# Kernel tuning notes

Measured on AMD Instinct MI355X. Metric: run time of the kernel, lower is better.

Reference implementation:

```python
import jax, jax.numpy as jnp
import numpy as np

N = 80000        # nodes
E = 1280000      # edges (avg degree 16)
D_IN, H1, H2, D_OUT = 64, 64, 64, 64


def _glorot(key, fan_in, fan_out):
    s = np.sqrt(6.0 / (fan_in + fan_out)).astype(np.float32)
    return jax.random.uniform(key, (fan_in, fan_out), jnp.float32, -s, s)


def setup_inputs() -> dict:
    key = jax.random.key(0)
    ks = jax.random.split(key, 5)
    X = jax.random.normal(ks[0], (N, D_IN), jnp.float32)
    edge_index = jax.random.randint(ks[1], (2, E), 0, N, dtype=jnp.int32).astype(jnp.int64)
    W1 = _glorot(ks[2], D_IN, H1)
    W2 = _glorot(ks[3], H1, H2)
    W3 = _glorot(ks[4], H2, D_OUT)
    b1 = jnp.zeros((H1,), jnp.float32)
    b2 = jnp.zeros((H2,), jnp.float32)
    b3 = jnp.zeros((D_OUT,), jnp.float32)
    return {"X": X, "edge_index": edge_index,
            "W1": W1, "b1": b1, "W2": W2, "b2": b2, "W3": W3, "b3": b3}


def _gcn_conv(x, W, b, src, dst, n):
    """PyG GCNConv: symmetric-normalized mean over A + I, then linear + bias.
    x' = D^{-1/2} (A + I) D^{-1/2} (x W) + b, deg counts self-loops."""
    x = x @ W                                   # [N, F_out]
    # in-degree including self loop (edge weights are 1)
    deg = jnp.ones((n,), x.dtype).at[dst].add(1.0)
    dinv = jax.lax.rsqrt(deg)                   # deg >= 1 always
    coef = dinv[src] * dinv[dst]                # [E]
    msg = x[src] * coef[:, None]                # [E, F_out] gather
    agg = jnp.zeros_like(x).at[dst].add(msg)    # scatter-add to targets
    agg = agg + x * (dinv * dinv)[:, None]      # self-loop contribution
    return agg + b


def reference(X, edge_index, W1, b1, W2, b2, W3, b3):
    src, dst = edge_index[0], edge_index[1]
    n = X.shape[0]
    h = jax.nn.relu(_gcn_conv(X, W1, b1, src, dst, n))
    h = jax.nn.relu(_gcn_conv(h, W2, b2, src, dst, n))
    out = _gcn_conv(h, W3, b3, src, dst, n)     # no activation on last layer
    return out
```

## Files before the change

kernel.cpp:

```cpp
#include <hip/hip_runtime.h>
#include <hip/hip_fp16.h>

#define NN 80000
#define NE 1280000
#define F  64
#define BSH 9
#define NB  157
#define CAP 12288
#define EPB 2560
#define EPT 10
#define PBLK (NE / EPB)

typedef _Float16 half_t;
typedef _Float16 half8 __attribute__((ext_vector_type(8)));
typedef float f32x4 __attribute__((ext_vector_type(4)));
typedef unsigned int uint_t;

__device__ __forceinline__ float2 h2f2(uint_t u) {
    __half2 h = *(__half2*)&u;
    return __half22float2(h);
}

__device__ __forceinline__ int ld_src(const int* __restrict__ idx, int e, int is64) {
    return is64 ? idx[2 * e] : idx[e];
}
__device__ __forceinline__ int ld_dst(const int* __restrict__ idx, int e, int is64) {
    return is64 ? idx[2 * NE + 2 * e] : idx[NE + e];
}

__global__ __launch_bounds__(256) void partition_kernel(
        const int* __restrict__ idx,
        int* __restrict__ bcur, int* __restrict__ ebuf) {
    __shared__ int cnt[NB];
    __shared__ int lbase[NB];
    __shared__ int gbase[NB];
    __shared__ int lds_val[EPB];
    __shared__ int lds_gaddr[EPB];
    __shared__ int is64_s;
    int tid = threadIdx.x;
    if (tid == 0) is64_s = 1;
    for (int i = tid; i < NB; i += 256) cnt[i] = 0;
    __syncthreads();
    if (idx[2 * tid + 1] != 0) is64_s = 0;
    __syncthreads();
    int is64 = is64_s;
    int e0 = blockIdx.x * EPB;
    int val[EPT], br[EPT];
    #pragma unroll
    for (int j = 0; j < EPT; ++j) {
        int e = e0 + j * 256 + tid;
        int s = ld_src(idx, e, is64);
        int d = ld_dst(idx, e, is64);
        int b = d >> BSH;
        val[j] = ((d & ((1 << BSH) - 1)) << 17) | s;
        int r = atomicAdd(&cnt[b], 1);
        br[j] = (b << 13) | r;
    }
    __syncthreads();
    if (tid < 64) {
        int carry = 0;
        for (int base = 0; base < NB; base += 64) {
            int i2 = base + tid;
            int v = (i2 < NB) ? cnt[i2] : 0;
            int incl = v;
            #pragma unroll
            for (int d2 = 1; d2 < 64; d2 <<= 1) {
                int t = __shfl_up(incl, d2, 64);
                if (tid >= d2) incl += t;
            }
            if (i2 < NB) lbase[i2] = carry + incl - v;
            carry += __shfl(incl, 63);
        }
    } else if (tid - 64 < NB) {
        int b = tid - 64;
        gbase[b] = atomicAdd(&bcur[b], cnt[b]);
    }
    __syncthreads();
    #pragma unroll
    for (int j = 0; j < EPT; ++j) {
        int b = br[j] >> 13, r = br[j] & 8191;
        int slot = lbase[b] + r;
        int g = gbase[b] + r;
        lds_val[slot]   = val[j];
        lds_gaddr[slot] = (g < CAP) ? (b * CAP + g) : -1;
    }
    __syncthreads();
    for (int i = tid; i < EPB; i += 256) {
        int a = lds_gaddr[i];
        if (a >= 0) ebuf[a] = lds_val[i];
    }
}

__global__ __launch_bounds__(512) void bucket_sort_kernel(
        const int* __restrict__ bcur, const int* __restrict__ ebuf,
        const float* __restrict__ X,
        int* __restrict__ edata, int* __restrict__ row_ptr,
        float* __restrict__ dinv, half_t* __restrict__ y0) {
    __shared__ int cnt[512];
    __shared__ int off[512];
    __shared__ int lds_out[CAP];
    __shared__ int ebase_s;
    int b = blockIdx.x, tid = threadIdx.x;
    cnt[tid] = 0;
    if (tid < 64) {
        int carry = 0;
        for (int base = 0; base < NB; base += 64) {
            int i2 = base + tid;
            int v = (i2 < NB) ? min(bcur[i2], CAP) : 0;
            int incl = v;
            #pragma unroll
            for (int d2 = 1; d2 < 64; d2 <<= 1) {
                int t = __shfl_up(incl, d2, 64);
                if (tid >= d2) incl += t;
            }
            if (i2 == b) ebase_s = carry + incl - v;
            carry += __shfl(incl, 63);
        }
    }
    __syncthreads();
    int bcnt = min(bcur[b], CAP);
    int ebase = ebase_s;
    const int* src = ebuf + b * CAP;
    for (int i = tid; i < bcnt; i += 512)
        atomicAdd(&cnt[src[i] >> 17], 1);
    __syncthreads();
    if (tid < 64) {
        int carry = 0;
        #pragma unroll
        for (int base = 0; base < 512; base += 64) {
            int v = cnt[base + tid];
            int incl = v;
            #pragma unroll
            for (int d2 = 1; d2 < 64; d2 <<= 1) {
                int t = __shfl_up(incl, d2, 64);
                if (tid >= d2) incl += t;
            }
            off[base + tid] = carry + incl - v;
            carry += __shfl(incl, 63);
        }
    }
    __syncthreads();
    int n0 = b << BSH;
    {
        int n = n0 + tid;
        if (n < NN) {
            row_ptr[n] = ebase + off[tid];
            dinv[n] = rsqrtf((float)cnt[tid] + 1.f);
        } else if (n == NN) {
            row_ptr[NN] = ebase + off[tid];
        }
    }
    __syncthreads();
    for (int j = tid; j < 512 * 16; j += 512) {
        int i = j >> 4, q = j & 15;
        int n = n0 + i;
        if (n >= NN) break;
        float dv = rsqrtf((float)cnt[i] + 1.f);
        float4 v = ((const float4*)(X + (size_t)n * F))[q];
        half_t h[4] = { (half_t)(v.x * dv), (half_t)(v.y * dv),
                        (half_t)(v.z * dv), (half_t)(v.w * dv) };
        ((uint2*)(y0 + (size_t)n * F))[q] = *(uint2*)h;
    }
    for (int i = tid; i < bcnt; i += 512) {
        int w = src[i];
        int pos = atomicAdd(&off[w >> 17], 1);
        lds_out[pos] = w & 0x1FFFF;
    }
    __syncthreads();
    for (int i = tid; i < bcnt; i += 512)
        edata[ebase + i] = lds_out[i];
}

__global__ __launch_bounds__(256) void gather_kernel(const half_t* __restrict__ y,
        const int* __restrict__ edata, const int* __restrict__ row_ptr,
        half_t* __restrict__ agg) {
    int n = blockIdx.x * 4 + (threadIdx.x >> 6);
    int lane = threadIdx.x & 63;
    int sub = lane >> 4, fl = lane & 15;
    int p0 = row_ptr[n], p1 = row_ptr[n + 1];
    float a0 = 0.f, a1 = 0.f, a2 = 0.f, a3 = 0.f;
    for (int base = p0; base < p1; base += 32) {
        int s[8]; float m[8];
        #pragma unroll
        for (int j = 0; j < 8; ++j) {
            int q = base + j * 4 + sub;
            int qc = q < p1 ? q : p1 - 1;
            s[j] = edata[qc];
            m[j] = (q < p1) ? 1.f : 0.f;
        }
        uint2 u[8];
        #pragma unroll
        for (int j = 0; j < 8; ++j)
            u[j] = ((const uint2*)(y + (size_t)s[j] * F))[fl];
        #pragma unroll
        for (int j = 0; j < 8; ++j) {
            float2 lo = h2f2(u[j].x), hi = h2f2(u[j].y);
            a0 = fmaf(m[j], lo.x, a0);
            a1 = fmaf(m[j], lo.y, a1);
            a2 = fmaf(m[j], hi.x, a2);
            a3 = fmaf(m[j], hi.y, a3);
        }
    }
    a0 += __shfl_down(a0, 32); a1 += __shfl_down(a1, 32);
    a2 += __shfl_down(a2, 32); a3 += __shfl_down(a3, 32);
    a0 += __shfl_down(a0, 16); a1 += __shfl_down(a1, 16);
    a2 += __shfl_down(a2, 16); a3 += __shfl_down(a3, 16);
    if (sub == 0) {
        float dv = rsqrtf((float)(p1 - p0) + 1.f);
        uint2 us = ((const uint2*)(y + (size_t)n * F))[fl];
        float2 slo = h2f2(us.x), shi = h2f2(us.y);
        half_t h[4] = { (half_t)(dv * (a0 + slo.x)), (half_t)(dv * (a1 + slo.y)),
                        (half_t)(dv * (a2 + shi.x)), (half_t)(dv * (a3 + shi.y)) };
        ((uint2*)(agg + (size_t)n * F))[fl] = *(uint2*)h;
    }
}

template <int RELU, int SCALE, int LAST>
__global__ __launch_bounds__(256) void gemm_mfma(
        const half_t* __restrict__ A, const float* __restrict__ W,
        const float* __restrict__ bias, const float* __restrict__ dinv,
        half_t* __restrict__ out_h, float* __restrict__ out_f32) {
    __shared__ half_t Wt[64][72];
    __shared__ half_t xt[128][72];
    int tid = threadIdx.x;
    for (int i = tid; i < 4096; i += 256) {
        int k = i >> 6, n2 = i & 63;
        Wt[n2][k] = (half_t)W[i];
    }
    int n0 = blockIdx.x * 128;
    for (int i2 = tid; i2 < 2048; i2 += 256) {
        int r = i2 >> 4, c = i2 & 15;
        ((uint2*)&xt[r][0])[c] = ((const uint2*)(A + (size_t)(n0 + r) * F))[c];
    }
    __syncthreads();
    int wv = tid >> 6, lane = tid & 63;
    int m = lane & 15, q = lane >> 4;
    #pragma unroll
    for (int rt = 0; rt < 2; ++rt) {
        int rbase = wv * 32 + rt * 16;
        const half_t* arow = &xt[rbase + m][q * 8];
        half8 A0 = *(const half8*)arow;
        half8 A1 = *(const half8*)(arow + 32);
        #pragma unroll
        for (int ct = 0; ct < 4; ++ct) {
            const half_t* brow = &Wt[ct * 16 + m][q * 8];
            half8 B0 = *(const half8*)brow;
            half8 B1 = *(const half8*)(brow + 32);
            f32x4 c = {0.f, 0.f, 0.f, 0.f};
            c = __builtin_amdgcn_mfma_f32_16x16x32_f16(A0, B0, c, 0, 0, 0);
            c = __builtin_amdgcn_mfma_f32_16x16x32_f16(A1, B1, c, 0, 0, 0);
            float bv = bias[ct * 16 + m];
            #pragma unroll
            for (int r = 0; r < 4; ++r) {
                int row = n0 + rbase + q * 4 + r;
                float v = c[r] + bv;
                if (RELU) v = fmaxf(v, 0.f);
                if (SCALE) v *= dinv[row];
                int col = ct * 16 + m;
                if (LAST) out_f32[(size_t)row * F + col] = v;
                else      out_h[(size_t)row * F + col] = (half_t)v;
            }
        }
    }
}

extern "C" void kernel_launch(void* const* d_in, const int* in_sizes, int n_in,
                              void* d_out, int out_size, void* d_ws, size_t ws_size,
                              hipStream_t stream) {
    const float* X  = (const float*)d_in[0];
    const int*  idx = (const int*)d_in[1];
    const float* W1 = (const float*)d_in[2];
    const float* b1 = (const float*)d_in[3];
    const float* W2 = (const float*)d_in[4];
    const float* b2 = (const float*)d_in[5];
    const float* W3 = (const float*)d_in[6];
    const float* b3 = (const float*)d_in[7];
    float* out = (float*)d_out;

    char* ws = (char*)d_ws;
    int*    bcur    = (int*)(ws + 256);
    int*    row_ptr = (int*)(ws + 1024);
    float*  dinv    = (float*)(ws + 321280);
    int*    edata   = (int*)(ws + 641536);
    half_t* ybufA   = (half_t*)(ws + 5761536);
    half_t* ybufB   = (half_t*)(ws + 16001536);
    int*    ebuf    = (int*)(ws + 26241536);

    hipMemsetAsync(bcur, 0, NB * sizeof(int), stream);
    partition_kernel<<<PBLK, 256, 0, stream>>>(idx, bcur, ebuf);
    bucket_sort_kernel<<<NB, 512, 0, stream>>>(bcur, ebuf, X, edata, row_ptr,
                                               dinv, ybufA);

    const int gBlocks = NN / 4;
    const int mBlocks = NN / 128;

    gather_kernel<<<gBlocks, 256, 0, stream>>>(ybufA, edata, row_ptr, ybufB);
    gemm_mfma<1, 1, 0><<<mBlocks, 256, 0, stream>>>(ybufB, W1, b1, dinv, ybufA, nullptr);
    gather_kernel<<<gBlocks, 256, 0, stream>>>(ybufA, edata, row_ptr, ybufB);
    gemm_mfma<1, 1, 0><<<mBlocks, 256, 0, stream>>>(ybufB, W2, b2, dinv, ybufA, nullptr);
    gather_kernel<<<gBlocks, 256, 0, stream>>>(ybufA, edata, row_ptr, ybufB);
    gemm_mfma<0, 0, 1><<<mBlocks, 256, 0, stream>>>(ybufB, W3, b3, dinv, nullptr, out);
}
```

Before: 257.1 us.

## Widen gather loads to 16 bytes, split X prescale into own kernel, enlarge partition chunks

The gather kernel now uses 8 lanes per neighbor row with 16-byte loads and 8 accumulators, so each pass covers 8 edges per load step instead of 4. This is meant to cut the number of load instructions per edge, at the cost of an extra shuffle-reduction step and more registers. The X prescale-to-fp16 is moved out of the 157-block bucket sort into a separate fully parallel kernel, trading an extra launch for better parallelism. The partition kernel also processes twice as many edges per block.

```diff
diff --git a/kernel.cpp b/kernel.cpp
--- a/kernel.cpp
+++ b/kernel.cpp
@@ -7,8 +7,8 @@
 #define BSH 9
 #define NB  157
 #define CAP 12288
-#define EPB 2560
-#define EPT 10
+#define EPB 5120
+#define EPT 20
 #define PBLK (NE / EPB)
 
 typedef _Float16 half_t;
@@ -93,9 +93,8 @@
 
 __global__ __launch_bounds__(512) void bucket_sort_kernel(
         const int* __restrict__ bcur, const int* __restrict__ ebuf,
-        const float* __restrict__ X,
         int* __restrict__ edata, int* __restrict__ row_ptr,
-        float* __restrict__ dinv, half_t* __restrict__ y0) {
+        float* __restrict__ dinv) {
     __shared__ int cnt[512];
     __shared__ int off[512];
     __shared__ int lds_out[CAP];
@@ -151,16 +150,6 @@
         }
     }
     __syncthreads();
-    for (int j = tid; j < 512 * 16; j += 512) {
-        int i = j >> 4, q = j & 15;
-        int n = n0 + i;
-        if (n >= NN) break;
-        float dv = rsqrtf((float)cnt[i] + 1.f);
-        float4 v = ((const float4*)(X + (size_t)n * F))[q];
-        half_t h[4] = { (half_t)(v.x * dv), (half_t)(v.y * dv),
-                        (half_t)(v.z * dv), (half_t)(v.w * dv) };
-        ((uint2*)(y0 + (size_t)n * F))[q] = *(uint2*)h;
-    }
     for (int i = tid; i < bcnt; i += 512) {
         int w = src[i];
         int pos = atomicAdd(&off[w >> 17], 1);
@@ -169,6 +158,18 @@
     __syncthreads();
     for (int i = tid; i < bcnt; i += 512)
         edata[ebase + i] = lds_out[i];
+}
+
+__global__ void prescale_kernel(const float* __restrict__ x, const float* __restrict__ dinv,
+                                half_t* __restrict__ y) {
+    int tid = blockIdx.x * blockDim.x + threadIdx.x;
+    if (tid >= NN * 16) return;
+    int n = tid >> 4, q = tid & 15;
+    float c = dinv[n];
+    float4 v = ((const float4*)(x + (size_t)n * F))[q];
+    half_t h[4] = { (half_t)(v.x * c), (half_t)(v.y * c),
+                    (half_t)(v.z * c), (half_t)(v.w * c) };
+    ((uint2*)(y + (size_t)n * F))[q] = *(uint2*)h;
 }
 
 __global__ __launch_bounds__(256) void gather_kernel(const half_t* __restrict__ y,
@@ -176,42 +177,51 @@
         half_t* __restrict__ agg) {
     int n = blockIdx.x * 4 + (threadIdx.x >> 6);
     int lane = threadIdx.x & 63;
-    int sub = lane >> 4, fl = lane & 15;
+    int sub = lane >> 3;
+    int fl  = lane & 7;
     int p0 = row_ptr[n], p1 = row_ptr[n + 1];
-    float a0 = 0.f, a1 = 0.f, a2 = 0.f, a3 = 0.f;
+    float a[8];
+    #pragma unroll
+    for (int i = 0; i < 8; ++i) a[i] = 0.f;
     for (int base = p0; base < p1; base += 32) {
-        int s[8]; float m[8];
-        #pragma unroll
-        for (int j = 0; j < 8; ++j) {
-            int q = base + j * 4 + sub;
+        int s[4]; float m[4];
+        #pragma unroll
+        for (int j = 0; j < 4; ++j) {
+            int q = base + j * 8 + sub;
             int qc = q < p1 ? q : p1 - 1;
             s[j] = edata[qc];
             m[j] = (q < p1) ? 1.f : 0.f;
         }
-        uint2 u[8];
-        #pragma unroll
-        for (int j = 0; j < 8; ++j)
-            u[j] = ((const uint2*)(y + (size_t)s[j] * F))[fl];
-        #pragma unroll
-        for (int j = 0; j < 8; ++j) {
-            float2 lo = h2f2(u[j].x), hi = h2f2(u[j].y);
-            a0 = fmaf(m[j], lo.x, a0);
-            a1 = fmaf(m[j], lo.y, a1);
-            a2 = fmaf(m[j], hi.x, a2);
-            a3 = fmaf(m[j], hi.y, a3);
-        }
-    }
-    a0 += __shfl_down(a0, 32); a1 += __shfl_down(a1, 32);
-    a2 += __shfl_down(a2, 32); a3 += __shfl_down(a3, 32);
-    a0 += __shfl_down(a0, 16); a1 += __shfl_down(a1, 16);
-    a2 += __shfl_down(a2, 16); a3 += __shfl_down(a3, 16);
+        uint4 u[4];
+        #pragma unroll
+        for (int j = 0; j < 4; ++j)
+            u[j] = ((const uint4*)(y + (size_t)s[j] * F))[fl];
+        #pragma unroll
+        for (int j = 0; j < 4; ++j) {
+            float2 f0 = h2f2(u[j].x), f1 = h2f2(u[j].y);
+            float2 f2 = h2f2(u[j].z), f3 = h2f2(u[j].w);
+            a[0] = fmaf(m[j], f0.x, a[0]); a[1] = fmaf(m[j], f0.y, a[1]);
+            a[2] = fmaf(m[j], f1.x, a[2]); a[3] = fmaf(m[j], f1.y, a[3]);
+            a[4] = fmaf(m[j], f2.x, a[4]); a[5] = fmaf(m[j], f2.y, a[5]);
+            a[6] = fmaf(m[j], f3.x, a[6]); a[7] = fmaf(m[j], f3.y, a[7]);
+        }
+    }
+    #pragma unroll
+    for (int i = 0; i < 8; ++i) {
+        a[i] += __shfl_down(a[i], 32);
+        a[i] += __shfl_down(a[i], 16);
+        a[i] += __shfl_down(a[i], 8);
+    }
     if (sub == 0) {
         float dv = rsqrtf((float)(p1 - p0) + 1.f);
-        uint2 us = ((const uint2*)(y + (size_t)n * F))[fl];
-        float2 slo = h2f2(us.x), shi = h2f2(us.y);
-        half_t h[4] = { (half_t)(dv * (a0 + slo.x)), (half_t)(dv * (a1 + slo.y)),
-                        (half_t)(dv * (a2 + shi.x)), (half_t)(dv * (a3 + shi.y)) };
-        ((uint2*)(agg + (size_t)n * F))[fl] = *(uint2*)h;
+        uint4 us = ((const uint4*)(y + (size_t)n * F))[fl];
+        float2 s0 = h2f2(us.x), s1 = h2f2(us.y), s2 = h2f2(us.z), s3 = h2f2(us.w);
+        half_t h[8] = {
+            (half_t)(dv * (a[0] + s0.x)), (half_t)(dv * (a[1] + s0.y)),
+            (half_t)(dv * (a[2] + s1.x)), (half_t)(dv * (a[3] + s1.y)),
+            (half_t)(dv * (a[4] + s2.x)), (half_t)(dv * (a[5] + s2.y)),
+            (half_t)(dv * (a[6] + s3.x)), (half_t)(dv * (a[7] + s3.y)) };
+        ((uint4*)(agg + (size_t)n * F))[fl] = *(uint4*)h;
     }
 }
 
@@ -288,8 +298,8 @@
 
     hipMemsetAsync(bcur, 0, NB * sizeof(int), stream);
     partition_kernel<<<PBLK, 256, 0, stream>>>(idx, bcur, ebuf);
-    bucket_sort_kernel<<<NB, 512, 0, stream>>>(bcur, ebuf, X, edata, row_ptr,
-                                               dinv, ybufA);
+    bucket_sort_kernel<<<NB, 512, 0, stream>>>(bcur, ebuf, edata, row_ptr, dinv);
+    prescale_kernel<<<(NN * 16) / 256, 256, 0, stream>>>(X, dinv, ybufA);
 
     const int gBlocks = NN / 4;
     const int mBlocks = NN / 128;
```

Result: faster. 236.3 us (-8.1%).
